# Kernel optimization log

Hardware: AMD Instinct MI355X
Metric: run time of the kernel (lower is better)

Reference implementation:

```python
import jax, jax.numpy as jnp
import numpy as np

N_HEADS = 8

def setup_inputs() -> dict:
    key = jax.random.key(0)
    ks = jax.random.split(key, 8)
    N, D, H = 20000, 16, 256
    scale = np.float32(0.02)
    return {
        "h": jax.random.normal(ks[0], (N, H), dtype=jnp.float32),
        "attention_mask": jnp.zeros((N,), dtype=jnp.float32),
        "neighbor_idx": jax.random.randint(ks[1], (N, D), 0, N, dtype=jnp.int32),
        "Wq": jax.random.normal(ks[2], (H, H), dtype=jnp.float32) * scale,
        "bq": jnp.zeros((H,), dtype=jnp.float32),
        "Wk": jax.random.normal(ks[3], (H, H), dtype=jnp.float32) * scale,
        "bk": jnp.zeros((H,), dtype=jnp.float32),
        "Wv": jax.random.normal(ks[4], (H, H), dtype=jnp.float32) * scale,
        "bv": jnp.zeros((H,), dtype=jnp.float32),
    }

def reference(h, attention_mask, neighbor_idx, Wq, bq, Wk, bk, Wv, bv):
    N, H = h.shape
    nh = N_HEADS
    dh = H // nh
    inv_sqrt_dh = np.float32(1.0 / np.sqrt(dh))
    # query from each node's own state: [N, nh, dh]
    q = (h @ Wq.T + bq).reshape(N, nh, dh)
    # gather neighbor mailbox: [N, D, H]
    nb = h[neighbor_idx]
    k = (nb @ Wk.T + bk).reshape(N, -1, nh, dh)  # [N, D, nh, dh]
    v = (nb @ Wv.T + bv).reshape(N, -1, nh, dh)
    # scores: [N, nh, D]
    scores = jnp.einsum('nhd,nkhd->nhk', q, k) * inv_sqrt_dh
    # additive mask gathered from source nodes, broadcast over heads
    scores = scores + attention_mask[neighbor_idx][:, None, :]
    probs = jax.nn.softmax(scores, axis=-1)
    # dropout prob = 0.0 (eval) -> identity
    ctx = jnp.einsum('nhk,nkhd->nhd', probs, v).reshape(N, H)
    return ctx
```

## Files before the change

### kernel.cpp

```cpp
#include <hip/hip_runtime.h>
#include <hip/hip_fp16.h>
#include <math.h>

#define HDIM 256
#define DNEIGH 16

typedef __attribute__((ext_vector_type(8))) short short8;
typedef __attribute__((ext_vector_type(4))) float f32x4;

static __device__ __forceinline__ unsigned short f2bf(float f) {
    unsigned int u = __float_as_uint(f);
    unsigned int r = (u + 0x7fffu + ((u >> 16) & 1u)) >> 16;
    return (unsigned short)r;
}
static __device__ __forceinline__ float bf_lo(unsigned int u) {
    return __uint_as_float(u << 16);
}
static __device__ __forceinline__ float bf_hi(unsigned int u) {
    return __uint_as_float(u & 0xffff0000u);
}

#if __has_builtin(__builtin_amdgcn_cvt_pk_fp8_f32)
static __device__ __forceinline__ unsigned char f2fp8(float v) {
    int pk = __builtin_amdgcn_cvt_pk_fp8_f32(v, v, 0, false);
    return (unsigned char)(pk & 0xff);
}
#else
static __device__ __forceinline__ unsigned char f2fp8(float v) {
    unsigned short h = __half_as_ushort(__float2half(v * (1.0f / 256.0f)));
    unsigned short mag = h & 0x7fffu;
    mag = (unsigned short)((mag + 0x40u) >> 7);
    if (mag > 0x7f) mag = 0x7f;
    return (unsigned char)(((h >> 8) & 0x80u) | mag);
}
#endif

#if __has_builtin(__builtin_amdgcn_cvt_f32_fp8)
#define FP8D(u, i) __builtin_amdgcn_cvt_f32_fp8((u), (i))
#else
static __device__ __forceinline__ float fp8_byte_dec(unsigned int b) {
    unsigned int hb = ((b & 0x80u) << 8) | ((b & 0x7fu) << 7);
    return __half2float(__ushort_as_half((unsigned short)hb)) * 256.0f;
}
#define FP8D(u, i) fp8_byte_dec(((u) >> ((i) * 8)) & 0xffu)
#endif

static __device__ __forceinline__ void async_copy16(const void* g, void* l) {
    __builtin_amdgcn_global_load_lds(
        (const __attribute__((address_space(1))) unsigned int*)g,
        (__attribute__((address_space(3))) unsigned int*)l, 16, 0, 0);
}

__global__ __launch_bounds__(256) void cvt_kernel(
    const float* __restrict__ h,
    const float* __restrict__ wq, const float* __restrict__ wk, const float* __restrict__ wv,
    unsigned short* __restrict__ hb,
    unsigned short* __restrict__ wqb, unsigned short* __restrict__ wkb, unsigned short* __restrict__ wvb,
    int nh4)
{
    int i = blockIdx.x * 256 + threadIdx.x;
    const int total = nh4 + 3 * 16384;
    if (i >= total) return;
    const float4* src; unsigned short* dst; int off;
    if (i < nh4) { src = (const float4*)h; dst = hb; off = i; }
    else {
        int j = i - nh4; int s = j >> 14; off = j & 16383;
        src = (s == 0) ? (const float4*)wq : (s == 1) ? (const float4*)wk : (const float4*)wv;
        dst = (s == 0) ? wqb : (s == 1) ? wkb : wvb;
    }
    float4 v = src[off];
    ushort4 o;
    o.x = f2bf(v.x); o.y = f2bf(v.y); o.z = f2bf(v.z); o.w = f2bf(v.w);
    *(ushort4*)&dst[off * 4] = o;
}

__global__ __launch_bounds__(256, 1) void qkv_mfma_kernel(
    const unsigned short* __restrict__ hb,
    const unsigned short* __restrict__ Wqb,
    const unsigned short* __restrict__ Wkb,
    const unsigned short* __restrict__ Wvb,
    const float* __restrict__ bq, const float* __restrict__ bk, const float* __restrict__ bv,
    unsigned short* __restrict__ Qb, unsigned char* __restrict__ K8,
    unsigned short* __restrict__ Vb,
    int N)
{
    __shared__ unsigned short Ws[128 * 256];
    __shared__ unsigned short As[2][64 * 256];

    const int t = threadIdx.x;
    const int lane = t & 63;
    const int wid = t >> 6;
    const int wo = wid >> 1;
    const int wn2 = wid & 1;
    const int o0 = blockIdx.y * 128;
    const int sel = o0 >> 8;
    const int wrow0 = o0 & 255;

    const unsigned short* __restrict__ W = (sel == 0) ? Wqb : (sel == 1) ? Wkb : Wvb;
    const float* __restrict__ bias = (sel == 0) ? bq : (sel == 1) ? bk : bv;

    const int ntiles = (N + 63) >> 6;
    const int BX = gridDim.x;

    const int p = lane & 31;
    const int rhalf = lane >> 5;

#pragma unroll
    for (int r = 0; r < 16; ++r) {
        int lr = wid * 32 + r * 2 + rhalf;
        int c = (p & ~7) | ((p ^ lr) & 7);
        const unsigned short* gp = &W[(size_t)(wrow0 + lr) * 256 + c * 8];
        async_copy16(gp, &Ws[(wid * 32 + r * 2) * 256]);
    }
    {
        int g0 = blockIdx.x * 64;
#pragma unroll
        for (int r = 0; r < 8; ++r) {
            int lr = wid * 16 + r * 2 + rhalf;
            int c = (p & ~7) | ((p ^ lr) & 7);
            const unsigned short* gp = &hb[(size_t)(g0 + lr) * 256 + c * 8];
            async_copy16(gp, &As[0][(wid * 16 + r * 2) * 256]);
        }
    }
    __syncthreads();

    short8 af[8][4];
#pragma unroll
    for (int ks = 0; ks < 8; ++ks)
#pragma unroll
        for (int i = 0; i < 4; ++i) {
            int m = wo * 64 + i * 16 + (lane & 15);
            int c = ks * 4 + (lane >> 4);
            int pos = (c & ~7) | ((c ^ m) & 7);
            af[ks][i] = *(const short8*)&Ws[m * 256 + pos * 8];
        }

    const float qscale = 0.17677669529663688f;

    int tile = blockIdx.x;
    for (int it = 0; tile < ntiles; ++it, tile += BX) {
        int cur = it & 1;
        int nxt = tile + BX;
        if (nxt < ntiles) {
            int g0 = nxt * 64;
#pragma unroll
            for (int r = 0; r < 8; ++r) {
                int lr = wid * 16 + r * 2 + rhalf;
                int c = (p & ~7) | ((p ^ lr) & 7);
                const unsigned short* gp = &hb[(size_t)(g0 + lr) * 256 + c * 8];
                async_copy16(gp, &As[cur ^ 1][(wid * 16 + r * 2) * 256]);
            }
        }

        f32x4 acc[4][2] = {};
#pragma unroll
        for (int ks = 0; ks < 8; ++ks) {
            short8 bf[2];
#pragma unroll
            for (int j = 0; j < 2; ++j) {
                int n = wn2 * 32 + j * 16 + (lane & 15);
                int c = ks * 4 + (lane >> 4);
                int pos = (c & ~7) | ((c ^ n) & 7);
                bf[j] = *(const short8*)&As[cur][n * 256 + pos * 8];
            }
#pragma unroll
            for (int i = 0; i < 4; ++i)
#pragma unroll
                for (int j = 0; j < 2; ++j)
                    acc[i][j] = __builtin_amdgcn_mfma_f32_16x16x32_bf16(af[ks][i], bf[j], acc[i][j], 0, 0, 0);
        }

        int nodeb = tile * 64;
#pragma unroll
        for (int i = 0; i < 4; ++i) {
            int ch = wrow0 + wo * 64 + i * 16 + (lane >> 4) * 4;
            float4 b4 = *(const float4*)&bias[ch];
#pragma unroll
            for (int j = 0; j < 2; ++j) {
                int node = nodeb + wn2 * 32 + j * 16 + (lane & 15);
                if (node < N) {
                    float v0 = acc[i][j][0] + b4.x;
                    float v1 = acc[i][j][1] + b4.y;
                    float v2 = acc[i][j][2] + b4.z;
                    float v3 = acc[i][j][3] + b4.w;
                    if (sel == 0) {
                        ushort4 o;
                        o.x = f2bf(v0 * qscale); o.y = f2bf(v1 * qscale);
                        o.z = f2bf(v2 * qscale); o.w = f2bf(v3 * qscale);
                        *(ushort4*)&Qb[(size_t)node * HDIM + ch] = o;
                    } else if (sel == 1) {
                        uchar4 o;
                        o.x = f2fp8(v0); o.y = f2fp8(v1); o.z = f2fp8(v2); o.w = f2fp8(v3);
                        *(uchar4*)&K8[(size_t)node * HDIM + ch] = o;
                    } else {
                        ushort4 o;
                        o.x = f2bf(v0); o.y = f2bf(v1); o.z = f2bf(v2); o.w = f2bf(v3);
                        *(ushort4*)&Vb[(size_t)node * HDIM + ch] = o;
                    }
                }
            }
        }
        __syncthreads();
    }
}

__global__ __launch_bounds__(256) void attn4_kernel(
    const unsigned short* __restrict__ Qb,
    const unsigned char* __restrict__ K8,
    const unsigned short* __restrict__ Vb,
    const float* __restrict__ mask,
    const int* __restrict__ nidx,
    float* __restrict__ out,
    int N)
{
    const int w = threadIdx.x >> 6;
    const int lane = threadIdx.x & 63;
    const int n = blockIdx.x * 4 + w;
    if (n >= N) return;

    int idl = nidx[(size_t)n * DNEIGH + (lane & 15)];
    float mskl = mask[idl];

    unsigned int kreg[DNEIGH];
    uint2 vreg[DNEIGH];
#pragma unroll
    for (int d = 0; d < DNEIGH; ++d) {
        int id = __builtin_amdgcn_readlane(idl, d);
        kreg[d] = *(const unsigned int*)&K8[(size_t)id * HDIM + lane * 4];
        vreg[d] = *(const uint2*)&Vb[(size_t)id * HDIM + lane * 4];
    }

    uint2 qu = *(const uint2*)&Qb[(size_t)n * HDIM + lane * 4];
    const float q0 = bf_lo(qu.x), q1 = bf_hi(qu.x);
    const float q2 = bf_lo(qu.y), q3 = bf_hi(qu.y);

    float e[DNEIGH];
    float s = 0.f;
#pragma unroll
    for (int d = 0; d < DNEIGH; ++d) {
        float pdot = q0 * FP8D(kreg[d], 0) + q1 * FP8D(kreg[d], 1)
                   + q2 * FP8D(kreg[d], 2) + q3 * FP8D(kreg[d], 3);
        pdot += __shfl_xor(pdot, 1);
        pdot += __shfl_xor(pdot, 2);
        pdot += __shfl_xor(pdot, 4);
        float mk = __int_as_float(__builtin_amdgcn_readlane(__float_as_int(mskl), d));
        e[d] = __expf(pdot + mk);
        s += e[d];
    }
    float rs = 1.f / s;

    float4 acc = make_float4(0.f, 0.f, 0.f, 0.f);
#pragma unroll
    for (int d = 0; d < DNEIGH; ++d) {
        float wgt = e[d] * rs;
        acc.x += wgt * bf_lo(vreg[d].x);
        acc.y += wgt * bf_hi(vreg[d].x);
        acc.z += wgt * bf_lo(vreg[d].y);
        acc.w += wgt * bf_hi(vreg[d].y);
    }
    *(float4*)&out[(size_t)n * HDIM + lane * 4] = acc;
}

extern "C" void kernel_launch(void* const* d_in, const int* in_sizes, int n_in,
                              void* d_out, int out_size, void* d_ws, size_t ws_size,
                              hipStream_t stream)
{
    const float* h    = (const float*)d_in[0];
    const float* mask = (const float*)d_in[1];
    const int*   nidx = (const int*)d_in[2];
    const float* Wq   = (const float*)d_in[3];
    const float* bq   = (const float*)d_in[4];
    const float* Wk   = (const float*)d_in[5];
    const float* bk   = (const float*)d_in[6];
    const float* Wv   = (const float*)d_in[7];
    const float* bv   = (const float*)d_in[8];

    const int N = in_sizes[0] / HDIM;

    char* ws = (char*)d_ws;
    unsigned short* Qbp = (unsigned short*)ws; ws += (size_t)N * HDIM * 2;
    unsigned short* Vbp = (unsigned short*)ws; ws += (size_t)N * HDIM * 2;
    unsigned short* hbp = (unsigned short*)ws; ws += (size_t)N * HDIM * 2;
    unsigned char*  K8p = (unsigned char*)ws;  ws += (size_t)N * HDIM;
    unsigned short* Wqb = (unsigned short*)ws; ws += 65536 * 2;
    unsigned short* Wkb = (unsigned short*)ws; ws += 65536 * 2;
    unsigned short* Wvb = (unsigned short*)ws;

    const int nh4 = (N * HDIM) / 4;
    const int total = nh4 + 3 * 16384;
    cvt_kernel<<<(total + 255) / 256, 256, 0, stream>>>(h, Wq, Wk, Wv, hbp, Wqb, Wkb, Wvb, nh4);

    dim3 g1(42, 6);
    qkv_mfma_kernel<<<g1, 256, 0, stream>>>(hbp, Wqb, Wkb, Wvb, bq, bk, bv, Qbp, K8p, Vbp, N);

    attn4_kernel<<<(N + 3) / 4, 256, 0, stream>>>(Qbp, K8p, Vbp, mask, nidx, (float*)d_out, N);
}
```

Before: 138.5 us.

## Fuse fp32-to-bf16 conversion into QKV GEMM and interleave K/V storage

```diff
diff --git a/kernel.cpp b/kernel.cpp
--- a/kernel.cpp
+++ b/kernel.cpp
@@ -20,10 +20,20 @@
     return __uint_as_float(u & 0xffff0000u);
 }
 
+static __device__ __forceinline__ short8 pack8(float4 a, float4 b) {
+    short8 o;
+    o[0] = (short)f2bf(a.x); o[1] = (short)f2bf(a.y);
+    o[2] = (short)f2bf(a.z); o[3] = (short)f2bf(a.w);
+    o[4] = (short)f2bf(b.x); o[5] = (short)f2bf(b.y);
+    o[6] = (short)f2bf(b.z); o[7] = (short)f2bf(b.w);
+    return o;
+}
+
 #if __has_builtin(__builtin_amdgcn_cvt_pk_fp8_f32)
-static __device__ __forceinline__ unsigned char f2fp8(float v) {
-    int pk = __builtin_amdgcn_cvt_pk_fp8_f32(v, v, 0, false);
-    return (unsigned char)(pk & 0xff);
+static __device__ __forceinline__ unsigned int fp8x4(float v0, float v1, float v2, float v3) {
+    int p = __builtin_amdgcn_cvt_pk_fp8_f32(v0, v1, 0, false);
+    p = __builtin_amdgcn_cvt_pk_fp8_f32(v2, v3, p, true);
+    return (unsigned int)p;
 }
 #else
 static __device__ __forceinline__ unsigned char f2fp8(float v) {
@@ -33,8 +43,15 @@
     if (mag > 0x7f) mag = 0x7f;
     return (unsigned char)(((h >> 8) & 0x80u) | mag);
 }
-#endif
-
+static __device__ __forceinline__ unsigned int fp8x4(float v0, float v1, float v2, float v3) {
+    return (unsigned int)f2fp8(v0) | ((unsigned int)f2fp8(v1) << 8) |
+           ((unsigned int)f2fp8(v2) << 16) | ((unsigned int)f2fp8(v3) << 24);
+}
+#endif
+
+#if __has_builtin(__builtin_amdgcn_cvt_pk_f32_fp8)
+#define HAVE_PK_DEC 1
+#endif
 #if __has_builtin(__builtin_amdgcn_cvt_f32_fp8)
 #define FP8D(u, i) __builtin_amdgcn_cvt_f32_fp8((u), (i))
 #else
@@ -45,120 +62,99 @@
 #define FP8D(u, i) fp8_byte_dec(((u) >> ((i) * 8)) & 0xffu)
 #endif
 
-static __device__ __forceinline__ void async_copy16(const void* g, void* l) {
-    __builtin_amdgcn_global_load_lds(
-        (const __attribute__((address_space(1))) unsigned int*)g,
-        (__attribute__((address_space(3))) unsigned int*)l, 16, 0, 0);
-}
-
-__global__ __launch_bounds__(256) void cvt_kernel(
+__global__ __launch_bounds__(256, 1) void qkv_fused_kernel(
     const float* __restrict__ h,
-    const float* __restrict__ wq, const float* __restrict__ wk, const float* __restrict__ wv,
-    unsigned short* __restrict__ hb,
-    unsigned short* __restrict__ wqb, unsigned short* __restrict__ wkb, unsigned short* __restrict__ wvb,
-    int nh4)
-{
-    int i = blockIdx.x * 256 + threadIdx.x;
-    const int total = nh4 + 3 * 16384;
-    if (i >= total) return;
-    const float4* src; unsigned short* dst; int off;
-    if (i < nh4) { src = (const float4*)h; dst = hb; off = i; }
-    else {
-        int j = i - nh4; int s = j >> 14; off = j & 16383;
-        src = (s == 0) ? (const float4*)wq : (s == 1) ? (const float4*)wk : (const float4*)wv;
-        dst = (s == 0) ? wqb : (s == 1) ? wkb : wvb;
-    }
-    float4 v = src[off];
-    ushort4 o;
-    o.x = f2bf(v.x); o.y = f2bf(v.y); o.z = f2bf(v.z); o.w = f2bf(v.w);
-    *(ushort4*)&dst[off * 4] = o;
-}
-
-__global__ __launch_bounds__(256, 1) void qkv_mfma_kernel(
-    const unsigned short* __restrict__ hb,
-    const unsigned short* __restrict__ Wqb,
-    const unsigned short* __restrict__ Wkb,
-    const unsigned short* __restrict__ Wvb,
+    const float* __restrict__ Wq, const float* __restrict__ Wk, const float* __restrict__ Wv,
     const float* __restrict__ bq, const float* __restrict__ bk, const float* __restrict__ bv,
-    unsigned short* __restrict__ Qb, unsigned char* __restrict__ K8,
-    unsigned short* __restrict__ Vb,
+    unsigned short* __restrict__ Qb, unsigned char* __restrict__ KV,
     int N)
 {
-    __shared__ unsigned short Ws[128 * 256];
     __shared__ unsigned short As[2][64 * 256];
 
     const int t = threadIdx.x;
     const int lane = t & 63;
     const int wid = t >> 6;
-    const int wo = wid >> 1;
-    const int wn2 = wid & 1;
-    const int o0 = blockIdx.y * 128;
-    const int sel = o0 >> 8;
-    const int wrow0 = o0 & 255;
-
-    const unsigned short* __restrict__ W = (sel == 0) ? Wqb : (sel == 1) ? Wkb : Wvb;
+    const int sel = blockIdx.y;
+
+    const float* __restrict__ W    = (sel == 0) ? Wq : (sel == 1) ? Wk : Wv;
     const float* __restrict__ bias = (sel == 0) ? bq : (sel == 1) ? bk : bv;
+    const float wscale = (sel == 0) ? 0.17677669529663688f : 1.0f;
 
     const int ntiles = (N + 63) >> 6;
     const int BX = gridDim.x;
 
-    const int p = lane & 31;
-    const int rhalf = lane >> 5;
-
-#pragma unroll
-    for (int r = 0; r < 16; ++r) {
-        int lr = wid * 32 + r * 2 + rhalf;
-        int c = (p & ~7) | ((p ^ lr) & 7);
-        const unsigned short* gp = &W[(size_t)(wrow0 + lr) * 256 + c * 8];
-        async_copy16(gp, &Ws[(wid * 32 + r * 2) * 256]);
-    }
-    {
-        int g0 = blockIdx.x * 64;
-#pragma unroll
-        for (int r = 0; r < 8; ++r) {
-            int lr = wid * 16 + r * 2 + rhalf;
-            int c = (p & ~7) | ((p ^ lr) & 7);
-            const unsigned short* gp = &hb[(size_t)(g0 + lr) * 256 + c * 8];
-            async_copy16(gp, &As[0][(wid * 16 + r * 2) * 256]);
-        }
-    }
+    const int srow = wid * 8 + (lane >> 3);
+    const int tc = lane & 7;
+
+    short8 af[8][4];
+#pragma unroll
+    for (int ks = 0; ks < 8; ++ks)
+#pragma unroll
+        for (int i = 0; i < 4; ++i) {
+            int m = wid * 64 + i * 16 + (lane & 15);
+            int cf = (ks * 4 + (lane >> 4)) * 8;
+            float4 a = *(const float4*)&W[(size_t)m * 256 + cf];
+            float4 b = *(const float4*)&W[(size_t)m * 256 + cf + 4];
+            a.x *= wscale; a.y *= wscale; a.z *= wscale; a.w *= wscale;
+            b.x *= wscale; b.y *= wscale; b.z *= wscale; b.w *= wscale;
+            af[ks][i] = pack8(a, b);
+        }
+
+    float4 b4[4];
+#pragma unroll
+    for (int i = 0; i < 4; ++i) {
+        int ch = wid * 64 + i * 16 + (lane >> 4) * 4;
+        float4 bb = *(const float4*)&bias[ch];
+        bb.x *= wscale; bb.y *= wscale; bb.z *= wscale; bb.w *= wscale;
+        b4[i] = bb;
+    }
+
+    float4 fa[16];
+
+    auto LOADA = [&](int tile0) {
+#pragma unroll
+        for (int s = 0; s < 2; ++s) {
+            int gr = tile0 * 64 + s * 32 + srow;
+            if (gr > N - 1) gr = N - 1;
+            const float* hrow = &h[(size_t)gr * 256];
+#pragma unroll
+            for (int k = 0; k < 4; ++k) {
+                fa[s * 8 + k * 2 + 0] = *(const float4*)&hrow[k * 64 + tc * 8];
+                fa[s * 8 + k * 2 + 1] = *(const float4*)&hrow[k * 64 + tc * 8 + 4];
+            }
+        }
+    };
+    auto WRITEA = [&](int buf) {
+#pragma unroll
+        for (int s = 0; s < 2; ++s) {
+            int r = s * 32 + srow;
+#pragma unroll
+            for (int k = 0; k < 4; ++k) {
+                int c = k * 8 + tc;
+                int pos = (c & ~7) | ((c ^ r) & 7);
+                *(short8*)&As[buf][r * 256 + pos * 8] =
+                    pack8(fa[s * 8 + k * 2], fa[s * 8 + k * 2 + 1]);
+            }
+        }
+    };
+
+    int tile = blockIdx.x;
+    if (tile < ntiles) { LOADA(tile); WRITEA(0); }
     __syncthreads();
 
-    short8 af[8][4];
-#pragma unroll
-    for (int ks = 0; ks < 8; ++ks)
-#pragma unroll
-        for (int i = 0; i < 4; ++i) {
-            int m = wo * 64 + i * 16 + (lane & 15);
-            int c = ks * 4 + (lane >> 4);
-            int pos = (c & ~7) | ((c ^ m) & 7);
-            af[ks][i] = *(const short8*)&Ws[m * 256 + pos * 8];
-        }
-
-    const float qscale = 0.17677669529663688f;
-
-    int tile = blockIdx.x;
     for (int it = 0; tile < ntiles; ++it, tile += BX) {
         int cur = it & 1;
-        int nxt = tile + BX;
-        if (nxt < ntiles) {
-            int g0 = nxt * 64;
-#pragma unroll
-            for (int r = 0; r < 8; ++r) {
-                int lr = wid * 16 + r * 2 + rhalf;
-                int c = (p & ~7) | ((p ^ lr) & 7);
-                const unsigned short* gp = &hb[(size_t)(g0 + lr) * 256 + c * 8];
-                async_copy16(gp, &As[cur ^ 1][(wid * 16 + r * 2) * 256]);
-            }
-        }
-
-        f32x4 acc[4][2] = {};
+        int nxt_tile = tile + BX;
+        bool havenext = nxt_tile < ntiles;
+        if (havenext) LOADA(nxt_tile);
+
+        f32x4 acc[4][4] = {};
 #pragma unroll
         for (int ks = 0; ks < 8; ++ks) {
-            short8 bf[2];
-#pragma unroll
-            for (int j = 0; j < 2; ++j) {
-                int n = wn2 * 32 + j * 16 + (lane & 15);
+            short8 bf[4];
+#pragma unroll
+            for (int j = 0; j < 4; ++j) {
+                int n = j * 16 + (lane & 15);
                 int c = ks * 4 + (lane >> 4);
                 int pos = (c & ~7) | ((c ^ n) & 7);
                 bf[j] = *(const short8*)&As[cur][n * 256 + pos * 8];
@@ -166,48 +162,46 @@
 #pragma unroll
             for (int i = 0; i < 4; ++i)
 #pragma unroll
-                for (int j = 0; j < 2; ++j)
-                    acc[i][j] = __builtin_amdgcn_mfma_f32_16x16x32_bf16(af[ks][i], bf[j], acc[i][j], 0, 0, 0);
+                for (int j = 0; j < 4; ++j)
+                    acc[i][j] = __builtin_amdgcn_mfma_f32_16x16x32_bf16(
+                        af[ks][i], bf[j], acc[i][j], 0, 0, 0);
         }
 
         int nodeb = tile * 64;
 #pragma unroll
         for (int i = 0; i < 4; ++i) {
-            int ch = wrow0 + wo * 64 + i * 16 + (lane >> 4) * 4;
-            float4 b4 = *(const float4*)&bias[ch];
-#pragma unroll
-            for (int j = 0; j < 2; ++j) {
-                int node = nodeb + wn2 * 32 + j * 16 + (lane & 15);
+            int ch = wid * 64 + i * 16 + (lane >> 4) * 4;
+#pragma unroll
+            for (int j = 0; j < 4; ++j) {
+                int node = nodeb + j * 16 + (lane & 15);
                 if (node < N) {
-                    float v0 = acc[i][j][0] + b4.x;
-                    float v1 = acc[i][j][1] + b4.y;
-                    float v2 = acc[i][j][2] + b4.z;
-                    float v3 = acc[i][j][3] + b4.w;
+                    float v0 = acc[i][j][0] + b4[i].x;
+                    float v1 = acc[i][j][1] + b4[i].y;
+                    float v2 = acc[i][j][2] + b4[i].z;
+                    float v3 = acc[i][j][3] + b4[i].w;
                     if (sel == 0) {
                         ushort4 o;
-                        o.x = f2bf(v0 * qscale); o.y = f2bf(v1 * qscale);
-                        o.z = f2bf(v2 * qscale); o.w = f2bf(v3 * qscale);
+                        o.x = f2bf(v0); o.y = f2bf(v1); o.z = f2bf(v2); o.w = f2bf(v3);
                         *(ushort4*)&Qb[(size_t)node * HDIM + ch] = o;
                     } else if (sel == 1) {
-                        uchar4 o;
-                        o.x = f2fp8(v0); o.y = f2fp8(v1); o.z = f2fp8(v2); o.w = f2fp8(v3);
-                        *(uchar4*)&K8[(size_t)node * HDIM + ch] = o;
+                        *(unsigned int*)&KV[(size_t)node * 768 + ch] = fp8x4(v0, v1, v2, v3);
                     } else {
                         ushort4 o;
                         o.x = f2bf(v0); o.y = f2bf(v1); o.z = f2bf(v2); o.w = f2bf(v3);
-                        *(ushort4*)&Vb[(size_t)node * HDIM + ch] = o;
+                        *(ushort4*)&KV[(size_t)node * 768 + 256 + (size_t)ch * 2] = o;
                     }
                 }
             }
         }
+
+        if (havenext) WRITEA(cur ^ 1);
         __syncthreads();
     }
 }
 
 __global__ __launch_bounds__(256) void attn4_kernel(
     const unsigned short* __restrict__ Qb,
-    const unsigned char* __restrict__ K8,
-    const unsigned short* __restrict__ Vb,
+    const unsigned char* __restrict__ KV,
     const float* __restrict__ mask,
     const int* __restrict__ nidx,
     float* __restrict__ out,
@@ -226,8 +220,9 @@
 #pragma unroll
     for (int d = 0; d < DNEIGH; ++d) {
         int id = __builtin_amdgcn_readlane(idl, d);
-        kreg[d] = *(const unsigned int*)&K8[(size_t)id * HDIM + lane * 4];
-        vreg[d] = *(const uint2*)&Vb[(size_t)id * HDIM + lane * 4];
+        const unsigned char* kv = &KV[(size_t)id * 768];
+        kreg[d] = *(const unsigned int*)(kv + lane * 4);
+        vreg[d] = *(const uint2*)(kv + 256 + lane * 8);
     }
 
     uint2 qu = *(const uint2*)&Qb[(size_t)n * HDIM + lane * 4];
@@ -238,8 +233,15 @@
     float s = 0.f;
 #pragma unroll
     for (int d = 0; d < DNEIGH; ++d) {
-        float pdot = q0 * FP8D(kreg[d], 0) + q1 * FP8D(kreg[d], 1)
-                   + q2 * FP8D(kreg[d], 2) + q3 * FP8D(kreg[d], 3);
+        float pdot;
+#ifdef HAVE_PK_DEC
+        auto k01 = __builtin_amdgcn_cvt_pk_f32_fp8((int)kreg[d], false);
+        auto k23 = __builtin_amdgcn_cvt_pk_f32_fp8((int)kreg[d], true);
+        pdot = q0 * k01[0] + q1 * k01[1] + q2 * k23[0] + q3 * k23[1];
+#else
+        pdot = q0 * FP8D(kreg[d], 0) + q1 * FP8D(kreg[d], 1)
+             + q2 * FP8D(kreg[d], 2) + q3 * FP8D(kreg[d], 3);
+#endif
         pdot += __shfl_xor(pdot, 1);
         pdot += __shfl_xor(pdot, 2);
         pdot += __shfl_xor(pdot, 4);
@@ -279,19 +281,10 @@
 
     char* ws = (char*)d_ws;
     unsigned short* Qbp = (unsigned short*)ws; ws += (size_t)N * HDIM * 2;
-    unsigned short* Vbp = (unsigned short*)ws; ws += (size_t)N * HDIM * 2;
-    unsigned short* hbp = (unsigned short*)ws; ws += (size_t)N * HDIM * 2;
-    unsigned char*  K8p = (unsigned char*)ws;  ws += (size_t)N * HDIM;
-    unsigned short* Wqb = (unsigned short*)ws; ws += 65536 * 2;
-    unsigned short* Wkb = (unsigned short*)ws; ws += 65536 * 2;
-    unsigned short* Wvb = (unsigned short*)ws;
-
-    const int nh4 = (N * HDIM) / 4;
-    const int total = nh4 + 3 * 16384;
-    cvt_kernel<<<(total + 255) / 256, 256, 0, stream>>>(h, Wq, Wk, Wv, hbp, Wqb, Wkb, Wvb, nh4);
-
-    dim3 g1(42, 6);
-    qkv_mfma_kernel<<<g1, 256, 0, stream>>>(hbp, Wqb, Wkb, Wvb, bq, bk, bv, Qbp, K8p, Vbp, N);
-
-    attn4_kernel<<<(N + 3) / 4, 256, 0, stream>>>(Qbp, K8p, Vbp, mask, nidx, (float*)d_out, N);
-}
+    unsigned char*  KVp = (unsigned char*)ws;
+
+    dim3 g1(84, 3);
+    qkv_fused_kernel<<<g1, 256, 0, stream>>>(h, Wq, Wk, Wv, bq, bk, bv, Qbp, KVp, N);
+
+    attn4_kernel<<<(N + 3) / 4, 256, 0, stream>>>(Qbp, KVp, mask, nidx, (float*)d_out, N);
+}
```

Result: no change. 141.0 us (+1.8%).

## Interleave fp8 K and bf16 V per node, use packed conversion instructions

Applied to the files above, without the earlier changes.

```diff
diff --git a/kernel.cpp b/kernel.cpp
--- a/kernel.cpp
+++ b/kernel.cpp
@@ -8,11 +8,6 @@
 typedef __attribute__((ext_vector_type(8))) short short8;
 typedef __attribute__((ext_vector_type(4))) float f32x4;
 
-static __device__ __forceinline__ unsigned short f2bf(float f) {
-    unsigned int u = __float_as_uint(f);
-    unsigned int r = (u + 0x7fffu + ((u >> 16) & 1u)) >> 16;
-    return (unsigned short)r;
-}
 static __device__ __forceinline__ float bf_lo(unsigned int u) {
     return __uint_as_float(u << 16);
 }
@@ -20,10 +15,17 @@
     return __uint_as_float(u & 0xffff0000u);
 }
 
+static __device__ __forceinline__ unsigned int cvtpk(float lo, float hi) {
+    unsigned int r;
+    asm("v_cvt_pk_bf16_f32 %0, %1, %2" : "=v"(r) : "v"(lo), "v"(hi));
+    return r;
+}
+
 #if __has_builtin(__builtin_amdgcn_cvt_pk_fp8_f32)
-static __device__ __forceinline__ unsigned char f2fp8(float v) {
-    int pk = __builtin_amdgcn_cvt_pk_fp8_f32(v, v, 0, false);
-    return (unsigned char)(pk & 0xff);
+static __device__ __forceinline__ unsigned int fp8x4(float v0, float v1, float v2, float v3) {
+    int p = __builtin_amdgcn_cvt_pk_fp8_f32(v0, v1, 0, false);
+    p = __builtin_amdgcn_cvt_pk_fp8_f32(v2, v3, p, true);
+    return (unsigned int)p;
 }
 #else
 static __device__ __forceinline__ unsigned char f2fp8(float v) {
@@ -33,8 +35,15 @@
     if (mag > 0x7f) mag = 0x7f;
     return (unsigned char)(((h >> 8) & 0x80u) | mag);
 }
+static __device__ __forceinline__ unsigned int fp8x4(float v0, float v1, float v2, float v3) {
+    return (unsigned int)f2fp8(v0) | ((unsigned int)f2fp8(v1) << 8) |
+           ((unsigned int)f2fp8(v2) << 16) | ((unsigned int)f2fp8(v3) << 24);
+}
 #endif
 
+#if __has_builtin(__builtin_amdgcn_cvt_pk_f32_fp8)
+#define HAVE_PK_DEC 1
+#endif
 #if __has_builtin(__builtin_amdgcn_cvt_f32_fp8)
 #define FP8D(u, i) __builtin_amdgcn_cvt_f32_fp8((u), (i))
 #else
@@ -62,16 +71,17 @@
     const int total = nh4 + 3 * 16384;
     if (i >= total) return;
     const float4* src; unsigned short* dst; int off;
+    float sc = 1.0f;
     if (i < nh4) { src = (const float4*)h; dst = hb; off = i; }
     else {
         int j = i - nh4; int s = j >> 14; off = j & 16383;
         src = (s == 0) ? (const float4*)wq : (s == 1) ? (const float4*)wk : (const float4*)wv;
         dst = (s == 0) ? wqb : (s == 1) ? wkb : wvb;
+        if (s == 0) sc = 0.17677669529663688f;
     }
     float4 v = src[off];
-    ushort4 o;
-    o.x = f2bf(v.x); o.y = f2bf(v.y); o.z = f2bf(v.z); o.w = f2bf(v.w);
-    *(ushort4*)&dst[off * 4] = o;
+    uint2 o = make_uint2(cvtpk(v.x * sc, v.y * sc), cvtpk(v.z * sc, v.w * sc));
+    *(uint2*)&dst[off * 4] = o;
 }
 
 __global__ __launch_bounds__(256, 1) void qkv_mfma_kernel(
@@ -80,8 +90,7 @@
     const unsigned short* __restrict__ Wkb,
     const unsigned short* __restrict__ Wvb,
     const float* __restrict__ bq, const float* __restrict__ bk, const float* __restrict__ bv,
-    unsigned short* __restrict__ Qb, unsigned char* __restrict__ K8,
-    unsigned short* __restrict__ Vb,
+    unsigned short* __restrict__ Qb, unsigned char* __restrict__ KV,
     int N)
 {
     __shared__ unsigned short Ws[128 * 256];
@@ -98,6 +107,7 @@
 
     const unsigned short* __restrict__ W = (sel == 0) ? Wqb : (sel == 1) ? Wkb : Wvb;
     const float* __restrict__ bias = (sel == 0) ? bq : (sel == 1) ? bk : bv;
+    const float bscale = (sel == 0) ? 0.17677669529663688f : 1.0f;
 
     const int ntiles = (N + 63) >> 6;
     const int BX = gridDim.x;
@@ -135,7 +145,14 @@
             af[ks][i] = *(const short8*)&Ws[m * 256 + pos * 8];
         }
 
-    const float qscale = 0.17677669529663688f;
+    float4 b4[4];
+#pragma unroll
+    for (int i = 0; i < 4; ++i) {
+        int ch = wrow0 + wo * 64 + i * 16 + (lane >> 4) * 4;
+        float4 bb = *(const float4*)&bias[ch];
+        bb.x *= bscale; bb.y *= bscale; bb.z *= bscale; bb.w *= bscale;
+        b4[i] = bb;
+    }
 
     int tile = blockIdx.x;
     for (int it = 0; tile < ntiles; ++it, tile += BX) {
@@ -174,28 +191,25 @@
 #pragma unroll
         for (int i = 0; i < 4; ++i) {
             int ch = wrow0 + wo * 64 + i * 16 + (lane >> 4) * 4;
-            float4 b4 = *(const float4*)&bias[ch];
+            int g  = ch >> 2;
 #pragma unroll
             for (int j = 0; j < 2; ++j) {
                 int node = nodeb + wn2 * 32 + j * 16 + (lane & 15);
                 if (node < N) {
-                    float v0 = acc[i][j][0] + b4.x;
-                    float v1 = acc[i][j][1] + b4.y;
-                    float v2 = acc[i][j][2] + b4.z;
-                    float v3 = acc[i][j][3] + b4.w;
+                    float v0 = acc[i][j][0] + b4[i].x;
+                    float v1 = acc[i][j][1] + b4[i].y;
+                    float v2 = acc[i][j][2] + b4[i].z;
+                    float v3 = acc[i][j][3] + b4[i].w;
                     if (sel == 0) {
-                        ushort4 o;
-                        o.x = f2bf(v0 * qscale); o.y = f2bf(v1 * qscale);
-                        o.z = f2bf(v2 * qscale); o.w = f2bf(v3 * qscale);
-                        *(ushort4*)&Qb[(size_t)node * HDIM + ch] = o;
+                        *(uint2*)&Qb[(size_t)node * HDIM + ch] =
+                            make_uint2(cvtpk(v0, v1), cvtpk(v2, v3));
                     } else if (sel == 1) {
-                        uchar4 o;
-                        o.x = f2fp8(v0); o.y = f2fp8(v1); o.z = f2fp8(v2); o.w = f2fp8(v3);
-                        *(uchar4*)&K8[(size_t)node * HDIM + ch] = o;
+                        *(unsigned int*)&KV[(size_t)node * 768 + g * 12] =
+                            fp8x4(v0, v1, v2, v3);
                     } else {
-                        ushort4 o;
-                        o.x = f2bf(v0); o.y = f2bf(v1); o.z = f2bf(v2); o.w = f2bf(v3);
-                        *(ushort4*)&Vb[(size_t)node * HDIM + ch] = o;
+                        unsigned char* pp = &KV[(size_t)node * 768 + g * 12 + 4];
+                        *(unsigned int*)pp       = cvtpk(v0, v1);
+                        *(unsigned int*)(pp + 4) = cvtpk(v2, v3);
                     }
                 }
             }
@@ -206,8 +220,7 @@
 
 __global__ __launch_bounds__(256) void attn4_kernel(
     const unsigned short* __restrict__ Qb,
-    const unsigned char* __restrict__ K8,
-    const unsigned short* __restrict__ Vb,
+    const unsigned char* __restrict__ KV,
     const float* __restrict__ mask,
     const int* __restrict__ nidx,
     float* __restrict__ out,
@@ -221,13 +234,14 @@
     int idl = nidx[(size_t)n * DNEIGH + (lane & 15)];
     float mskl = mask[idl];
 
-    unsigned int kreg[DNEIGH];
-    uint2 vreg[DNEIGH];
+    unsigned int ka[DNEIGH], vb[DNEIGH], vc[DNEIGH];
 #pragma unroll
     for (int d = 0; d < DNEIGH; ++d) {
         int id = __builtin_amdgcn_readlane(idl, d);
-        kreg[d] = *(const unsigned int*)&K8[(size_t)id * HDIM + lane * 4];
-        vreg[d] = *(const uint2*)&Vb[(size_t)id * HDIM + lane * 4];
+        const unsigned char* p = &KV[(size_t)id * 768 + lane * 12];
+        ka[d] = *(const unsigned int*)p;
+        vb[d] = *(const unsigned int*)(p + 4);
+        vc[d] = *(const unsigned int*)(p + 8);
     }
 
     uint2 qu = *(const uint2*)&Qb[(size_t)n * HDIM + lane * 4];
@@ -238,8 +252,15 @@
     float s = 0.f;
 #pragma unroll
     for (int d = 0; d < DNEIGH; ++d) {
-        float pdot = q0 * FP8D(kreg[d], 0) + q1 * FP8D(kreg[d], 1)
-                   + q2 * FP8D(kreg[d], 2) + q3 * FP8D(kreg[d], 3);
+        float pdot;
+#ifdef HAVE_PK_DEC
+        auto k01 = __builtin_amdgcn_cvt_pk_f32_fp8((int)ka[d], false);
+        auto k23 = __builtin_amdgcn_cvt_pk_f32_fp8((int)ka[d], true);
+        pdot = q0 * k01[0] + q1 * k01[1] + q2 * k23[0] + q3 * k23[1];
+#else
+        pdot = q0 * FP8D(ka[d], 0) + q1 * FP8D(ka[d], 1)
+             + q2 * FP8D(ka[d], 2) + q3 * FP8D(ka[d], 3);
+#endif
         pdot += __shfl_xor(pdot, 1);
         pdot += __shfl_xor(pdot, 2);
         pdot += __shfl_xor(pdot, 4);
@@ -253,10 +274,10 @@
 #pragma unroll
     for (int d = 0; d < DNEIGH; ++d) {
         float wgt = e[d] * rs;
-        acc.x += wgt * bf_lo(vreg[d].x);
-        acc.y += wgt * bf_hi(vreg[d].x);
-        acc.z += wgt * bf_lo(vreg[d].y);
-        acc.w += wgt * bf_hi(vreg[d].y);
+        acc.x += wgt * bf_lo(vb[d]);
+        acc.y += wgt * bf_hi(vb[d]);
+        acc.z += wgt * bf_lo(vc[d]);
+        acc.w += wgt * bf_hi(vc[d]);
     }
     *(float4*)&out[(size_t)n * HDIM + lane * 4] = acc;
 }
@@ -279,9 +300,8 @@
 
     char* ws = (char*)d_ws;
     unsigned short* Qbp = (unsigned short*)ws; ws += (size_t)N * HDIM * 2;
-    unsigned short* Vbp = (unsigned short*)ws; ws += (size_t)N * HDIM * 2;
     unsigned short* hbp = (unsigned short*)ws; ws += (size_t)N * HDIM * 2;
-    unsigned char*  K8p = (unsigned char*)ws;  ws += (size_t)N * HDIM;
+    unsigned char*  KVp = (unsigned char*)ws;  ws += (size_t)N * 768;
     unsigned short* Wqb = (unsigned short*)ws; ws += 65536 * 2;
     unsigned short* Wkb = (unsigned short*)ws; ws += 65536 * 2;
     unsigned short* Wvb = (unsigned short*)ws;
@@ -291,7 +311,7 @@
     cvt_kernel<<<(total + 255) / 256, 256, 0, stream>>>(h, Wq, Wk, Wv, hbp, Wqb, Wkb, Wvb, nh4);
 
     dim3 g1(42, 6);
-    qkv_mfma_kernel<<<g1, 256, 0, stream>>>(hbp, Wqb, Wkb, Wvb, bq, bk, bv, Qbp, K8p, Vbp, N);
-
-    attn4_kernel<<<(N + 3) / 4, 256, 0, stream>>>(Qbp, K8p, Vbp, mask, nidx, (float*)d_out, N);
-}
+    qkv_mfma_kernel<<<g1, 256, 0, stream>>>(hbp, Wqb, Wkb, Wvb, bq, bk, bv, Qbp, KVp, N);
+
+    attn4_kernel<<<(N + 3) / 4, 256, 0, stream>>>(Qbp, KVp, mask, nidx, (float*)d_out, N);
+}
```

Measured after the change: 142.9 us. 3.2% more time.
